# Optimization experiments

Measured on AMD Instinct MI355X. Metric: run time of the kernel, lower is better.

Reference implementation:

```python
import jax, jax.numpy as jnp
import numpy as np

B, S, D, H = 2, 2048, 1024, 16
HD = D // H          # head_dim = 64
HALF = HD // 2       # rotary pair count = 32


def rope_freqs(seq_len, half, base=10000.0):
    # Llama-style: theta_j = base^(-2j/head_dim), angle m*theta_j
    inv = 1.0 / (base ** (np.arange(0, half, dtype=np.float32) / half))
    ang = np.arange(seq_len, dtype=np.float32)[:, None] * inv[None, :]  # [S, half]
    return jnp.asarray(np.cos(ang)), jnp.asarray(np.sin(ang))


def setup_inputs() -> dict:
    key = jax.random.key(0)
    kx, kq, kk, kv, ko = jax.random.split(key, 5)
    cos, sin = rope_freqs(S, HALF)  # real/imag of m_theta_polar_tensor
    s = 0.02
    return {
        "x": jax.random.normal(kx, (B, S, D), dtype=jnp.float32),
        "freqs_cos": cos,
        "freqs_sin": sin,
        "Wq": jax.random.normal(kq, (D, D), dtype=jnp.float32) * s,
        "Wk": jax.random.normal(kk, (D, D), dtype=jnp.float32) * s,
        "Wv": jax.random.normal(kv, (D, D), dtype=jnp.float32) * s,
        "Wout": jax.random.normal(ko, (D, D), dtype=jnp.float32) * s,
    }


def _apply_rope(t, cos, sin):
    # t: [B, S, H, HD]; rotate consecutive pairs (complex multiply)
    b, s, h, hd = t.shape
    tr = t.reshape(b, s, h, hd // 2, 2)
    t0, t1 = tr[..., 0], tr[..., 1]
    c = cos[None, :, None, :]  # [1, S, 1, HALF]
    sn = sin[None, :, None, :]
    o0 = t0 * c - t1 * sn
    o1 = t0 * sn + t1 * c
    return jnp.stack([o0, o1], axis=-1).reshape(b, s, h, hd)


def reference(x, freqs_cos, freqs_sin, Wq, Wk, Wv, Wout):
    b, s, _ = x.shape
    q = (x @ Wq).reshape(b, s, H, HD)
    k = (x @ Wk).reshape(b, s, H, HD)
    v = (x @ Wv).reshape(b, s, H, HD)
    q = _apply_rope(q, freqs_cos, freqs_sin)
    k = _apply_rope(k, freqs_cos, freqs_sin)
    # [B, H, S, S]
    scores = jnp.einsum("bqhd,bkhd->bhqk", q, k) / jnp.sqrt(jnp.float32(HD))
    causal = jnp.triu(jnp.ones((s, s), dtype=bool), k=1)
    scores = jnp.where(causal[None, None], -jnp.inf, scores)
    weights = jax.nn.softmax(scores, axis=-1)
    vectors = jnp.einsum("bhqk,bkhd->bqhd", weights, v).reshape(b, s, D)
    return vectors @ Wout
```

## Files before the change

kernel.cpp:

```cpp
#include <hip/hip_runtime.h>
#include <stdint.h>

typedef unsigned short u16;
typedef __attribute__((ext_vector_type(8))) short short8;
typedef __attribute__((ext_vector_type(4))) short short4v;
typedef __attribute__((ext_vector_type(4))) float f32x4;
typedef __attribute__((ext_vector_type(4))) unsigned short ushort4v;
typedef __attribute__((ext_vector_type(2))) unsigned int uint2v;

#define NB 2
#define NS 2048
#define ND 1024
#define NH 16
#define HDIM 64
#define NHALF 32
#define QSCALE 0.18033688f
#define NEGBIG -3.0e38f

__device__ __forceinline__ float bf2f(u16 u) {
  union { unsigned u; float f; } v; v.u = ((unsigned)u) << 16; return v.f;
}
__device__ __forceinline__ u16 f2bf(float f) {
  union { float f; unsigned u; } v; v.f = f;
  unsigned r = v.u + 0x7fffu + ((v.u >> 16) & 1u);
  return (u16)(r >> 16);
}

__device__ __forceinline__ unsigned cvt_pk_bf16(float lo, float hi) {
  unsigned r;
  asm("v_cvt_pk_bf16_f32 %0, %1, %2" : "=v"(r) : "v"(lo), "v"(hi));
  return r;
}

__device__ __forceinline__ void gld_lds16(const u16* g, u16* l) {
  void* gv = (void*)g;
  __builtin_amdgcn_global_load_lds((__attribute__((address_space(1))) void*)gv,
                                   (__attribute__((address_space(3))) void*)l, 16, 0, 0);
}

__global__ void cvt_x(const float* __restrict__ x, u16* __restrict__ xb) {
  int i = blockIdx.x * 256 + threadIdx.x;
  float4 v = ((const float4*)x)[i];
  ushort4v o;
  o.x = f2bf(v.x); o.y = f2bf(v.y); o.z = f2bf(v.z); o.w = f2bf(v.w);
  ((ushort4v*)xb)[i] = o;
}

__global__ void transpose_w3(const float* __restrict__ W0, const float* __restrict__ W1,
                             const float* __restrict__ W2, u16* __restrict__ dst0) {
  __shared__ float tile[32][33];
  const int z = blockIdx.z;
  const float* W = (z == 0) ? W0 : (z == 1) ? W1 : W2;
  u16* dst = dst0 + (size_t)z * ND * ND;
  const int n0 = blockIdx.x * 32, k0 = blockIdx.y * 32;
  const int tx = threadIdx.x, ty = threadIdx.y;
#pragma unroll
  for (int i = 0; i < 4; ++i)
    tile[ty + i * 8][tx] = W[(size_t)(k0 + ty + i * 8) * ND + n0 + tx];
  __syncthreads();
#pragma unroll
  for (int i = 0; i < 4; ++i)
    dst[(size_t)(n0 + ty + i * 8) * ND + k0 + tx] = f2bf(tile[tx][ty + i * 8]);
}

__global__ void transpose_w(const float* __restrict__ W, u16* __restrict__ dst) {
  __shared__ float tile[32][33];
  const int n0 = blockIdx.x * 32, k0 = blockIdx.y * 32;
  const int tx = threadIdx.x, ty = threadIdx.y;
#pragma unroll
  for (int i = 0; i < 4; ++i)
    tile[ty + i * 8][tx] = W[(size_t)(k0 + ty + i * 8) * ND + n0 + tx];
  __syncthreads();
#pragma unroll
  for (int i = 0; i < 4; ++i)
    dst[(size_t)(n0 + ty + i * 8) * ND + k0 + tx] = f2bf(tile[tx][ty + i * 8]);
}

__global__ void transpose_v(const u16* __restrict__ Vb, u16* __restrict__ VT) {
  __shared__ u16 tile[64][72];
  const int bh = blockIdx.y, s0 = blockIdx.x << 6;
  const int tid = threadIdx.x;
  const u16* src = Vb + ((size_t)bh * NS + s0) * HDIM;
  u16* dst = VT + (size_t)bh * HDIM * NS + s0;
#pragma unroll
  for (int it = 0; it < 2; ++it) {
    int i = it * 256 + tid;
    int s = i >> 3, d0 = (i & 7) << 3;
    *(short8*)&tile[s][d0] = *(const short8*)(src + (size_t)s * HDIM + d0);
  }
  __syncthreads();
#pragma unroll
  for (int it = 0; it < 2; ++it) {
    int i = it * 256 + tid;
    int d = i >> 3, ss0 = (i & 7) << 3;
    short8 v;
#pragma unroll
    for (int e = 0; e < 8; ++e) v[e] = tile[ss0 + e][d];
    *(short8*)(dst + (size_t)d * NS + ss0) = v;
  }
}

template<int MODE>
__global__ __launch_bounds__(256) void gemm_bt(
    const u16* __restrict__ A, const u16* __restrict__ BT,
    u16* __restrict__ qo, u16* __restrict__ ko, u16* __restrict__ vo,
    float* __restrict__ fo) {
  __shared__ u16 smem[8192];
  const int tid = threadIdx.x;
  const int w = tid >> 6, lane = tid & 63;
  const int lr = lane & 15, lg = lane >> 4;
  const int bm = blockIdx.y << 7, bn = blockIdx.x << 7;
  const int wr = (w >> 1) << 6, wc = (w & 1) << 6;
  f32x4 acc[4][4] = {};

  for (int kt = 0; kt < ND; kt += 32) {
#pragma unroll
    for (int r = 0; r < 2; ++r) {
      const int idx = ((r << 2) + w) * 64 + lane;
      const int row = idx >> 2, ch = (idx & 3) << 3;
      gld_lds16(A + (size_t)(bm + row) * ND + kt + ch, smem + ((r << 2) + w) * 512);
      gld_lds16(BT + (size_t)(bn + row) * ND + kt + ch, smem + 4096 + ((r << 2) + w) * 512);
    }
    __syncthreads();
    short8 af[4], bfr[4];
#pragma unroll
    for (int mi = 0; mi < 4; ++mi)
      af[mi] = *(const short8*)(smem + (wr + mi * 16 + lr) * 32 + lg * 8);
#pragma unroll
    for (int ni = 0; ni < 4; ++ni)
      bfr[ni] = *(const short8*)(smem + 4096 + (wc + ni * 16 + lr) * 32 + lg * 8);
#pragma unroll
    for (int mi = 0; mi < 4; ++mi)
#pragma unroll
      for (int ni = 0; ni < 4; ++ni)
        acc[mi][ni] = __builtin_amdgcn_mfma_f32_16x16x32_bf16(af[mi], bfr[ni], acc[mi][ni], 0, 0, 0);
    __syncthreads();
  }

  if (MODE == 0) {
#pragma unroll
    for (int mi = 0; mi < 4; ++mi) {
#pragma unroll
      for (int ni = 0; ni < 4; ++ni) {
        const int n = bn + wc + ni * 16 + lr;
        const int which = n >> 10, hh = (n >> 6) & 15, d = n & 63;
        u16* dst = which == 0 ? qo : which == 1 ? ko : vo;
#pragma unroll
        for (int j = 0; j < 4; ++j) {
          const int m = bm + wr + mi * 16 + (lg << 2) + j;
          const int b = m >> 11, s = m & 2047;
          dst[(((size_t)(b * NH + hh) * NS + s) << 6) + d] = f2bf(acc[mi][ni][j]);
        }
      }
    }
  } else {
#pragma unroll
    for (int mi = 0; mi < 4; ++mi)
#pragma unroll
      for (int ni = 0; ni < 4; ++ni)
#pragma unroll
        for (int j = 0; j < 4; ++j) {
          const int m = bm + wr + mi * 16 + (lg << 2) + j;
          const int n = bn + wc + ni * 16 + lr;
          fo[(size_t)m * ND + n] = acc[mi][ni][j];
        }
  }
}

__global__ void rope_k(u16* __restrict__ Qb, u16* __restrict__ Kb,
                       const float* __restrict__ cosT, const float* __restrict__ sinT) {
  int t = blockIdx.x * 256 + threadIdx.x;
  int g = t & 7;
  int s = (t >> 3) & 2047;
  int bh = t >> 14;
  float4 c4 = *(const float4*)(cosT + s * NHALF + (g << 2));
  float4 s4 = *(const float4*)(sinT + s * NHALF + (g << 2));
  size_t off = (((size_t)bh * NS + s) << 6) + (g << 3);
  short8 q = *(const short8*)(Qb + off);
  short8 k = *(const short8*)(Kb + off);
  float cc[4] = {c4.x, c4.y, c4.z, c4.w}, ss[4] = {s4.x, s4.y, s4.z, s4.w};
  short8 qo, ko;
#pragma unroll
  for (int p = 0; p < 4; ++p) {
    float q0 = bf2f((u16)q[2 * p]), q1 = bf2f((u16)q[2 * p + 1]);
    qo[2 * p]     = (short)f2bf((q0 * cc[p] - q1 * ss[p]) * QSCALE);
    qo[2 * p + 1] = (short)f2bf((q0 * ss[p] + q1 * cc[p]) * QSCALE);
    float k0 = bf2f((u16)k[2 * p]), k1 = bf2f((u16)k[2 * p + 1]);
    ko[2 * p]     = (short)f2bf(k0 * cc[p] - k1 * ss[p]);
    ko[2 * p + 1] = (short)f2bf(k0 * ss[p] + k1 * cc[p]);
  }
  *(short8*)(Qb + off) = qo;
  *(short8*)(Kb + off) = ko;
}

__global__ __launch_bounds__(256, 4) void attn_k(
    const u16* __restrict__ Qb, const u16* __restrict__ Kb,
    const u16* __restrict__ VT, u16* __restrict__ Ob) {
  __shared__ u16 K2[2][4096];
  __shared__ u16 V2[2][4096];
  __shared__ u16 Pl[4][1024];
  const int tid = threadIdx.x, w = tid >> 6, lane = tid & 63;
  const int lr = lane & 15, lg = lane >> 4;
  const int bid = blockIdx.x;
  const int xcd = bid & 7, i = bid >> 3;
  const int bh = xcd * 4 + (i & 3);
  const int pair = i >> 2;
  const int b = bh >> 4, h = bh & 15;
  const u16* Qp = Qb + (size_t)bh * NS * HDIM;
  const u16* Kp = Kb + (size_t)bh * NS * HDIM;
  const u16* Vp = VT + (size_t)bh * NS * HDIM;

  int kf_off[4][2], vb_off[4][2], pw_off[4], pa_off[2];
#pragma unroll
  for (int u = 0; u < 4; ++u) {
    const int kvr = (u << 4) + lr;
#pragma unroll
    for (int c = 0; c < 2; ++c)
      kf_off[u][c] = kvr * 64 + ((((c << 6) + (lg << 4)) ^ ((kvr & 7) << 4)) >> 1);
  }
#pragma unroll
  for (int dn = 0; dn < 4; ++dn) {
    const int d = (dn << 4) + lr;
#pragma unroll
    for (int ks = 0; ks < 2; ++ks)
      vb_off[dn][ks] = d * 64 + ((((ks << 6) + (lg << 4)) ^ ((d & 7) << 4)) >> 1);
  }
#pragma unroll
  for (int u = 0; u < 4; ++u)
    pw_off[u] = lr * 64 + ((((u << 5) + (lg << 3)) ^ ((lr & 7) << 4)) >> 1);
#pragma unroll
  for (int ks = 0; ks < 2; ++ks)
    pa_off[ks] = lr * 64 + ((((ks << 6) + (lg << 4)) ^ ((lr & 7) << 4)) >> 1);
  u16* Pw = &Pl[w][0];

  const int rr = tid >> 3, slot = tid & 7;
  const int soff = (((slot << 4) ^ ((rr & 7) << 4)) >> 1);
  const u16* kg0 = Kp + rr * HDIM + soff;
  const u16* kg1 = Kp + (rr + 32) * HDIM + soff;
  const u16* vg0 = Vp + (size_t)rr * NS + soff;
  const u16* vg1 = Vp + (size_t)(rr + 32) * NS + soff;

#define STAGE(BUFI, KV0)                                         \
  {                                                              \
    gld_lds16(kg0 + (KV0) * HDIM, &K2[BUFI][w * 512]);           \
    gld_lds16(kg1 + (KV0) * HDIM, &K2[BUFI][(4 + w) * 512]);     \
    gld_lds16(vg0 + (KV0),        &V2[BUFI][w * 512]);           \
    gld_lds16(vg1 + (KV0),        &V2[BUFI][(4 + w) * 512]);     \
  }

#define STEP(BUF, KVT)                                                            \
  {                                                                               \
    const int kv0 = (KVT) << 6;                                                   \
    if ((KVT) + 1 < nst) STAGE(BUF ^ 1, kv0 + 64);                                \
    const u16* Kl = K2[BUF];                                                      \
    const u16* Vl = V2[BUF];                                                      \
    f32x4 st[4] = {};                                                             \
    __builtin_amdgcn_s_setprio(1);                                                \
    _Pragma("unroll") for (int u = 0; u < 4; ++u)                                 \
      _Pragma("unroll") for (int c = 0; c < 2; ++c)                               \
        st[u] = __builtin_amdgcn_mfma_f32_16x16x32_bf16(                          \
            *(const short8*)(Kl + kf_off[u][c]), qf[c], st[u], 0, 0, 0);          \
    __builtin_amdgcn_s_setprio(0);                                                \
    if (kv0 + 63 > qw) {                                                          \
      _Pragma("unroll") for (int u = 0; u < 4; ++u)                               \
        _Pragma("unroll") for (int j = 0; j < 4; ++j) {                           \
          const int kvg = kv0 + (u << 4) + (lg << 2) + j;                         \
          if (kvg > q_col) st[u][j] = NEGBIG;                                     \
        }                                                                         \
    }                                                                             \
    _Pragma("unroll") for (int u = 0; u < 4; ++u) {                               \
      const float e0 = __builtin_amdgcn_exp2f(st[u][0]);                          \
      const float e1 = __builtin_amdgcn_exp2f(st[u][1]);                          \
      const float e2 = __builtin_amdgcn_exp2f(st[u][2]);                          \
      const float e3 = __builtin_amdgcn_exp2f(st[u][3]);                          \
      lacc += (e0 + e1) + (e2 + e3);                                              \
      uint2v pk;                                                                  \
      pk.x = cvt_pk_bf16(e0, e1);                                                 \
      pk.y = cvt_pk_bf16(e2, e3);                                                 \
      *(uint2v*)(Pw + pw_off[u]) = pk;                                            \
    }                                                                             \
    {                                                                             \
      short8 pa0 = *(const short8*)(Pw + pa_off[0]);                              \
      short8 pa1 = *(const short8*)(Pw + pa_off[1]);                              \
      __builtin_amdgcn_s_setprio(1);                                              \
      _Pragma("unroll") for (int dn = 0; dn < 4; ++dn) {                          \
        o[dn] = __builtin_amdgcn_mfma_f32_16x16x32_bf16(                          \
            pa0, *(const short8*)(Vl + vb_off[dn][0]), o[dn], 0, 0, 0);           \
        o[dn] = __builtin_amdgcn_mfma_f32_16x16x32_bf16(                          \
            pa1, *(const short8*)(Vl + vb_off[dn][1]), o[dn], 0, 0, 0);           \
      }                                                                           \
      __builtin_amdgcn_s_setprio(0);                                              \
    }                                                                             \
    __syncthreads();                                                              \
  }

  for (int seg = 0; seg < 2; ++seg) {
    const int tile = seg ? pair : 31 - pair;
    const int q0 = tile << 6;
    const int qw = q0 + w * 16;
    const int q_col = qw + lr;
    const int nst = tile + 1;

    short8 qf[2];
#pragma unroll
    for (int c = 0; c < 2; ++c)
      qf[c] = *(const short8*)(Qp + (size_t)(qw + lr) * HDIM + c * 32 + lg * 8);

    f32x4 o[4] = {};
    float lacc = 0.f;

    STAGE(0, 0);
    __syncthreads();

    int kvt = 0;
    for (; kvt + 2 <= nst; kvt += 2) {
      STEP(0, kvt);
      STEP(1, kvt + 1);
    }
    if (kvt < nst) STEP(0, kvt);

    float rs = lacc;
    rs += __shfl_xor(rs, 16);
    rs += __shfl_xor(rs, 32);
    float li[4];
#pragma unroll
    for (int j = 0; j < 4; ++j) li[j] = 1.0f / __shfl(rs, (lg << 2) + j);
#pragma unroll
    for (int dn = 0; dn < 4; ++dn)
#pragma unroll
      for (int j = 0; j < 4; ++j) {
        const int m = b * NS + qw + (lg << 2) + j;
        const int col = h * 64 + dn * 16 + lr;
        Ob[(size_t)m * ND + col] = f2bf(o[dn][j] * li[j]);
      }
  }
}

extern "C" void kernel_launch(void* const* d_in, const int* in_sizes, int n_in,
                              void* d_out, int out_size, void* d_ws, size_t ws_size,
                              hipStream_t stream) {
  const float* x  = (const float*)d_in[0];
  const float* fc = (const float*)d_in[1];
  const float* fs = (const float*)d_in[2];
  const float* Wq = (const float*)d_in[3];
  const float* Wk = (const float*)d_in[4];
  const float* Wv = (const float*)d_in[5];
  const float* Wo = (const float*)d_in[6];
  float* out = (float*)d_out;
  char* ws = (char*)d_ws;

  u16* xb    = (u16*)(ws);
  u16* WTqkv = (u16*)(ws + (size_t)(8u << 20));
  u16* VT    = (u16*)(ws + (size_t)(8u << 20));
  u16* Qb    = (u16*)(ws + (size_t)(16u << 20));
  u16* Kb    = (u16*)(ws + (size_t)(24u << 20));
  u16* Vb    = (u16*)(ws + (size_t)(32u << 20));
  u16* WTo   = (u16*)(ws + (size_t)(32u << 20));
  u16* Ob    = xb;

  cvt_x<<<4096, 256, 0, stream>>>(x, xb);
  transpose_w3<<<dim3(32, 32, 3), dim3(32, 8), 0, stream>>>(Wq, Wk, Wv, WTqkv);
  gemm_bt<0><<<dim3(24, 32), 256, 0, stream>>>(xb, WTqkv, Qb, Kb, Vb, nullptr);
  rope_k<<<2048, 256, 0, stream>>>(Qb, Kb, fc, fs);
  transpose_v<<<dim3(32, 32), 256, 0, stream>>>(Vb, VT);
  transpose_w<<<dim3(32, 32), dim3(32, 8), 0, stream>>>(Wo, WTo);
  attn_k<<<512, 256, 0, stream>>>(Qb, Kb, VT, Ob);
  gemm_bt<1><<<dim3(8, 32), 256, 0, stream>>>(Ob, WTo, nullptr, nullptr, nullptr, out);
}
```

Baseline: 120.3 us.

## Fuse RoPE into QKV GEMM epilogue and double-buffer the output GEMM

Moves the rotary embedding and Q scaling into the QKV GEMM epilogue. Accumulators are staged through shared memory so each lane writes 16 contiguous bf16 values with vector stores, and the separate rope kernel, with its extra read and write of Q and K, goes away. The output projection becomes its own kernel with 512 threads, double-buffered LDS loads that prefetch the next K tile during the MFMAs, and raised wave priority around the MFMA block. The costs are extra LDS use and a shared-memory round trip in the epilogue. Q/K are now rounded to bf16 once after RoPE rather than twice, which slightly changes numerics.

Result: slower. 126.7 us (+5.3%).

```diff
diff --git a/kernel.cpp b/kernel.cpp
--- a/kernel.cpp
+++ b/kernel.cpp
@@ -7,6 +7,7 @@
 typedef __attribute__((ext_vector_type(4))) float f32x4;
 typedef __attribute__((ext_vector_type(4))) unsigned short ushort4v;
 typedef __attribute__((ext_vector_type(2))) unsigned int uint2v;
+typedef __attribute__((ext_vector_type(4))) unsigned int uint4v;
 
 #define NB 2
 #define NS 2048
@@ -100,12 +101,12 @@
   }
 }
 
-template<int MODE>
-__global__ __launch_bounds__(256) void gemm_bt(
+__global__ __launch_bounds__(256) void gemm_qkv(
     const u16* __restrict__ A, const u16* __restrict__ BT,
     u16* __restrict__ qo, u16* __restrict__ ko, u16* __restrict__ vo,
-    float* __restrict__ fo) {
+    const float* __restrict__ cosT, const float* __restrict__ sinT) {
   __shared__ u16 smem[8192];
+  __shared__ float epi[4][16][68];
   const int tid = threadIdx.x;
   const int w = tid >> 6, lane = tid & 63;
   const int lr = lane & 15, lg = lane >> 4;
@@ -137,60 +138,107 @@
     __syncthreads();
   }
 
-  if (MODE == 0) {
-#pragma unroll
-    for (int mi = 0; mi < 4; ++mi) {
-#pragma unroll
-      for (int ni = 0; ni < 4; ++ni) {
+  const int er = lane >> 2;
+  const int ec = lane & 3;
+  const int n0 = bn + wc + (ec << 4);
+  const int which = n0 >> 10, hh = (n0 >> 6) & 15, d0 = n0 & 63;
+  u16* dstv = which == 0 ? qo : which == 1 ? ko : vo;
+  const int i0 = d0 >> 1;
+  const float sc = which == 0 ? QSCALE : 1.0f;
+
+#pragma unroll
+  for (int mi = 0; mi < 4; ++mi) {
+#pragma unroll
+    for (int ni = 0; ni < 4; ++ni)
+#pragma unroll
+      for (int j = 0; j < 4; ++j)
+        epi[w][(lg << 2) + j][ni * 16 + lr] = acc[mi][ni][j];
+    const int m = bm + wr + mi * 16 + er;
+    const int b = m >> 11, s = m & 2047;
+    float v[16];
+#pragma unroll
+    for (int c = 0; c < 4; ++c)
+      *(f32x4*)(v + c * 4) = *(const f32x4*)(&epi[w][er][(ec << 4) + c * 4]);
+    unsigned pk[8];
+    if (which < 2) {
+      const float4 c0 = *(const float4*)(cosT + s * NHALF + i0);
+      const float4 c1 = *(const float4*)(cosT + s * NHALF + i0 + 4);
+      const float4 s0 = *(const float4*)(sinT + s * NHALF + i0);
+      const float4 s1 = *(const float4*)(sinT + s * NHALF + i0 + 4);
+      const float cc[8] = {c0.x, c0.y, c0.z, c0.w, c1.x, c1.y, c1.z, c1.w};
+      const float ss[8] = {s0.x, s0.y, s0.z, s0.w, s1.x, s1.y, s1.z, s1.w};
+#pragma unroll
+      for (int p = 0; p < 8; ++p) {
+        const float o0 = (v[2 * p] * cc[p] - v[2 * p + 1] * ss[p]) * sc;
+        const float o1 = (v[2 * p] * ss[p] + v[2 * p + 1] * cc[p]) * sc;
+        pk[p] = cvt_pk_bf16(o0, o1);
+      }
+    } else {
+#pragma unroll
+      for (int p = 0; p < 8; ++p)
+        pk[p] = cvt_pk_bf16(v[2 * p], v[2 * p + 1]);
+    }
+    u16* dp = dstv + (((size_t)(b * NH + hh) * NS + s) << 6) + d0;
+    uint4v o0, o1;
+    o0.x = pk[0]; o0.y = pk[1]; o0.z = pk[2]; o0.w = pk[3];
+    o1.x = pk[4]; o1.y = pk[5]; o1.z = pk[6]; o1.w = pk[7];
+    *(uint4v*)dp = o0;
+    *(uint4v*)(dp + 8) = o1;
+  }
+}
+
+__global__ __launch_bounds__(512) void gemm_out(
+    const u16* __restrict__ A, const u16* __restrict__ BT, float* __restrict__ fo) {
+  __shared__ u16 smem[2][8192];
+  const int tid = threadIdx.x, w = tid >> 6, lane = tid & 63;
+  const int lr = lane & 15, lg = lane >> 4;
+  const int bm = blockIdx.y << 7, bn = blockIdx.x << 7;
+  const int wr = (w >> 2) << 6, wc = (w & 3) << 5;
+  f32x4 acc[4][2] = {};
+  const u16* ag = A + (size_t)(bm + w * 16 + (lane >> 2)) * ND + ((lane & 3) << 3);
+  const u16* bg = BT + (size_t)(bn + w * 16 + (lane >> 2)) * ND + ((lane & 3) << 3);
+
+#define GSTAGE(BUF, KT)                                  \
+  {                                                      \
+    gld_lds16(ag + (KT), &smem[BUF][w * 512]);           \
+    gld_lds16(bg + (KT), &smem[BUF][4096 + w * 512]);    \
+  }
+
+  GSTAGE(0, 0);
+  __syncthreads();
+  int cur = 0;
+  for (int kt = 0; kt < ND; kt += 32) {
+    if (kt + 32 < ND) GSTAGE(cur ^ 1, kt + 32);
+    const u16* As = smem[cur];
+    const u16* Bs = smem[cur] + 4096;
+    short8 af[4], bf[2];
+#pragma unroll
+    for (int mi = 0; mi < 4; ++mi)
+      af[mi] = *(const short8*)(As + (wr + mi * 16 + lr) * 32 + lg * 8);
+#pragma unroll
+    for (int ni = 0; ni < 2; ++ni)
+      bf[ni] = *(const short8*)(Bs + (wc + ni * 16 + lr) * 32 + lg * 8);
+    __builtin_amdgcn_s_setprio(1);
+#pragma unroll
+    for (int mi = 0; mi < 4; ++mi)
+#pragma unroll
+      for (int ni = 0; ni < 2; ++ni)
+        acc[mi][ni] = __builtin_amdgcn_mfma_f32_16x16x32_bf16(af[mi], bf[ni], acc[mi][ni], 0, 0, 0);
+    __builtin_amdgcn_s_setprio(0);
+    __syncthreads();
+    cur ^= 1;
+  }
+
+#pragma unroll
+  for (int mi = 0; mi < 4; ++mi)
+#pragma unroll
+    for (int ni = 0; ni < 2; ++ni)
+#pragma unroll
+      for (int j = 0; j < 4; ++j) {
+        const int m = bm + wr + mi * 16 + (lg << 2) + j;
         const int n = bn + wc + ni * 16 + lr;
-        const int which = n >> 10, hh = (n >> 6) & 15, d = n & 63;
-        u16* dst = which == 0 ? qo : which == 1 ? ko : vo;
-#pragma unroll
-        for (int j = 0; j < 4; ++j) {
-          const int m = bm + wr + mi * 16 + (lg << 2) + j;
-          const int b = m >> 11, s = m & 2047;
-          dst[(((size_t)(b * NH + hh) * NS + s) << 6) + d] = f2bf(acc[mi][ni][j]);
-        }
+        fo[(size_t)m * ND + n] = acc[mi][ni][j];
       }
-    }
-  } else {
-#pragma unroll
-    for (int mi = 0; mi < 4; ++mi)
-#pragma unroll
-      for (int ni = 0; ni < 4; ++ni)
-#pragma unroll
-        for (int j = 0; j < 4; ++j) {
-          const int m = bm + wr + mi * 16 + (lg << 2) + j;
-          const int n = bn + wc + ni * 16 + lr;
-          fo[(size_t)m * ND + n] = acc[mi][ni][j];
-        }
-  }
-}
-
-__global__ void rope_k(u16* __restrict__ Qb, u16* __restrict__ Kb,
-                       const float* __restrict__ cosT, const float* __restrict__ sinT) {
-  int t = blockIdx.x * 256 + threadIdx.x;
-  int g = t & 7;
-  int s = (t >> 3) & 2047;
-  int bh = t >> 14;
-  float4 c4 = *(const float4*)(cosT + s * NHALF + (g << 2));
-  float4 s4 = *(const float4*)(sinT + s * NHALF + (g << 2));
-  size_t off = (((size_t)bh * NS + s) << 6) + (g << 3);
-  short8 q = *(const short8*)(Qb + off);
-  short8 k = *(const short8*)(Kb + off);
-  float cc[4] = {c4.x, c4.y, c4.z, c4.w}, ss[4] = {s4.x, s4.y, s4.z, s4.w};
-  short8 qo, ko;
-#pragma unroll
-  for (int p = 0; p < 4; ++p) {
-    float q0 = bf2f((u16)q[2 * p]), q1 = bf2f((u16)q[2 * p + 1]);
-    qo[2 * p]     = (short)f2bf((q0 * cc[p] - q1 * ss[p]) * QSCALE);
-    qo[2 * p + 1] = (short)f2bf((q0 * ss[p] + q1 * cc[p]) * QSCALE);
-    float k0 = bf2f((u16)k[2 * p]), k1 = bf2f((u16)k[2 * p + 1]);
-    ko[2 * p]     = (short)f2bf(k0 * cc[p] - k1 * ss[p]);
-    ko[2 * p + 1] = (short)f2bf(k0 * ss[p] + k1 * cc[p]);
-  }
-  *(short8*)(Qb + off) = qo;
-  *(short8*)(Kb + off) = ko;
 }
 
 __global__ __launch_bounds__(256, 4) void attn_k(
@@ -360,10 +408,9 @@
 
   cvt_x<<<4096, 256, 0, stream>>>(x, xb);
   transpose_w3<<<dim3(32, 32, 3), dim3(32, 8), 0, stream>>>(Wq, Wk, Wv, WTqkv);
-  gemm_bt<0><<<dim3(24, 32), 256, 0, stream>>>(xb, WTqkv, Qb, Kb, Vb, nullptr);
-  rope_k<<<2048, 256, 0, stream>>>(Qb, Kb, fc, fs);
+  gemm_qkv<<<dim3(24, 32), 256, 0, stream>>>(xb, WTqkv, Qb, Kb, Vb, fc, fs);
   transpose_v<<<dim3(32, 32), 256, 0, stream>>>(Vb, VT);
   transpose_w<<<dim3(32, 32), dim3(32, 8), 0, stream>>>(Wo, WTo);
   attn_k<<<512, 256, 0, stream>>>(Qb, Kb, VT, Ob);
-  gemm_bt<1><<<dim3(8, 32), 256, 0, stream>>>(Ob, WTo, nullptr, nullptr, nullptr, out);
-}
+  gemm_out<<<dim3(8, 32), 512, 0, stream>>>(Ob, WTo, out);
+}
```

## Rework bf16 GEMMs with K=64 tiles, XOR-swizzled LDS, and smaller output-projection tiles

Applied to the files above, without the earlier changes.

The GEMM kernel now stages 64-wide K slices instead of 32, which halves the number of barrier pairs per tile. LDS rows are XOR-swizzled so the fragment reads avoid bank conflicts, and fragment offsets are precomputed outside the loop. The M tile becomes a template parameter. The output projection uses 64-row tiles, doubling its grid to 512 blocks for better CU occupancy on the 256-CU part, at the cost of less B-tile reuse. LDS use per block grows, which may lower occupancy.

Measured after the change: 107.7 us. -10.4%, faster.

```diff
diff --git a/kernel.cpp b/kernel.cpp
--- a/kernel.cpp
+++ b/kernel.cpp
@@ -100,46 +100,67 @@
   }
 }
 
-template<int MODE>
-__global__ __launch_bounds__(256) void gemm_bt(
+template<int MI, int MODE>
+__global__ __launch_bounds__(256) void gemm64(
     const u16* __restrict__ A, const u16* __restrict__ BT,
     u16* __restrict__ qo, u16* __restrict__ ko, u16* __restrict__ vo,
     float* __restrict__ fo) {
-  __shared__ u16 smem[8192];
+  __shared__ u16 smem[MI * 2048 + 8192];
   const int tid = threadIdx.x;
   const int w = tid >> 6, lane = tid & 63;
   const int lr = lane & 15, lg = lane >> 4;
-  const int bm = blockIdx.y << 7, bn = blockIdx.x << 7;
-  const int wr = (w >> 1) << 6, wc = (w & 1) << 6;
-  f32x4 acc[4][4] = {};
-
-  for (int kt = 0; kt < ND; kt += 32) {
-#pragma unroll
-    for (int r = 0; r < 2; ++r) {
-      const int idx = ((r << 2) + w) * 64 + lane;
-      const int row = idx >> 2, ch = (idx & 3) << 3;
-      gld_lds16(A + (size_t)(bm + row) * ND + kt + ch, smem + ((r << 2) + w) * 512);
-      gld_lds16(BT + (size_t)(bn + row) * ND + kt + ch, smem + 4096 + ((r << 2) + w) * 512);
+  const int bm = blockIdx.y * (MI * 32), bn = blockIdx.x << 7;
+  const int wr = (w >> 1) * (MI * 16), wc = (w & 1) << 6;
+  f32x4 acc[MI][4] = {};
+
+  const int arow = tid >> 3;
+  const int aslot = (tid & 7) ^ (arow & 7);
+  const u16* ags = A + (size_t)(bm + arow) * ND + (aslot << 3);
+  const u16* bgs = BT + (size_t)(bn + arow) * ND + (aslot << 3);
+  u16* const As = smem;
+  u16* const Bs = smem + MI * 2048;
+
+  int af_off[MI][2], bf_off[4][2];
+#pragma unroll
+  for (int mi = 0; mi < MI; ++mi)
+#pragma unroll
+    for (int kk = 0; kk < 2; ++kk)
+      af_off[mi][kk] = (wr + mi * 16 + lr) * 64 + ((((kk << 2) + lg) ^ (lr & 7)) << 3);
+#pragma unroll
+  for (int ni = 0; ni < 4; ++ni)
+#pragma unroll
+    for (int kk = 0; kk < 2; ++kk)
+      bf_off[ni][kk] = (wc + ni * 16 + lr) * 64 + ((((kk << 2) + lg) ^ (lr & 7)) << 3);
+
+  for (int kt = 0; kt < ND; kt += 64) {
+#pragma unroll
+    for (int it = 0; it < MI; ++it)
+      gld_lds16(ags + it * (32 * ND) + kt, As + it * 2048 + w * 512);
+#pragma unroll
+    for (int it = 0; it < 4; ++it)
+      gld_lds16(bgs + it * (32 * ND) + kt, Bs + it * 2048 + w * 512);
+    __syncthreads();
+#pragma unroll
+    for (int kk = 0; kk < 2; ++kk) {
+      short8 af[MI], bfr[4];
+#pragma unroll
+      for (int mi = 0; mi < MI; ++mi)
+        af[mi] = *(const short8*)(As + af_off[mi][kk]);
+#pragma unroll
+      for (int ni = 0; ni < 4; ++ni)
+        bfr[ni] = *(const short8*)(Bs + bf_off[ni][kk]);
+#pragma unroll
+      for (int mi = 0; mi < MI; ++mi)
+#pragma unroll
+        for (int ni = 0; ni < 4; ++ni)
+          acc[mi][ni] = __builtin_amdgcn_mfma_f32_16x16x32_bf16(af[mi], bfr[ni], acc[mi][ni], 0, 0, 0);
     }
     __syncthreads();
-    short8 af[4], bfr[4];
-#pragma unroll
-    for (int mi = 0; mi < 4; ++mi)
-      af[mi] = *(const short8*)(smem + (wr + mi * 16 + lr) * 32 + lg * 8);
-#pragma unroll
-    for (int ni = 0; ni < 4; ++ni)
-      bfr[ni] = *(const short8*)(smem + 4096 + (wc + ni * 16 + lr) * 32 + lg * 8);
-#pragma unroll
-    for (int mi = 0; mi < 4; ++mi)
-#pragma unroll
-      for (int ni = 0; ni < 4; ++ni)
-        acc[mi][ni] = __builtin_amdgcn_mfma_f32_16x16x32_bf16(af[mi], bfr[ni], acc[mi][ni], 0, 0, 0);
-    __syncthreads();
   }
 
   if (MODE == 0) {
 #pragma unroll
-    for (int mi = 0; mi < 4; ++mi) {
+    for (int mi = 0; mi < MI; ++mi) {
 #pragma unroll
       for (int ni = 0; ni < 4; ++ni) {
         const int n = bn + wc + ni * 16 + lr;
@@ -155,7 +176,7 @@
     }
   } else {
 #pragma unroll
-    for (int mi = 0; mi < 4; ++mi)
+    for (int mi = 0; mi < MI; ++mi)
 #pragma unroll
       for (int ni = 0; ni < 4; ++ni)
 #pragma unroll
@@ -360,10 +381,10 @@
 
   cvt_x<<<4096, 256, 0, stream>>>(x, xb);
   transpose_w3<<<dim3(32, 32, 3), dim3(32, 8), 0, stream>>>(Wq, Wk, Wv, WTqkv);
-  gemm_bt<0><<<dim3(24, 32), 256, 0, stream>>>(xb, WTqkv, Qb, Kb, Vb, nullptr);
+  gemm64<4, 0><<<dim3(24, 32), 256, 0, stream>>>(xb, WTqkv, Qb, Kb, Vb, nullptr);
   rope_k<<<2048, 256, 0, stream>>>(Qb, Kb, fc, fs);
   transpose_v<<<dim3(32, 32), 256, 0, stream>>>(Vb, VT);
   transpose_w<<<dim3(32, 32), dim3(32, 8), 0, stream>>>(Wo, WTo);
   attn_k<<<512, 256, 0, stream>>>(Qb, Kb, VT, Ob);
-  gemm_bt<1><<<dim3(8, 32), 256, 0, stream>>>(Ob, WTo, nullptr, nullptr, nullptr, out);
-}
+  gemm64<2, 1><<<dim3(8, 64), 256, 0, stream>>>(Ob, WTo, nullptr, nullptr, nullptr, out);
+}
```
